# Performance work log

Hardware: AMD Instinct MI355X
Metric: run time of the kernel (lower is better)

## Reference

```python
import jax, jax.numpy as jnp
import numpy as np
import math

B, T, TE, D, H = 1, 2048, 1024, 1024, 16
HD = D // H
INF = 1e9  # infinity_proxy from the original module
INIT_SCALE = 0.02


def sinusoid_pos_emb(timesteps, dim):
    # Transformer-XL sinusoids for relative positions [timesteps-1 .. 0].
    inv_freq = 1.0 / (10000.0 ** (np.arange(0, dim, 2) / dim))
    pos_seq = np.arange(timesteps - 1, -1, -1.0)
    inp = np.einsum('i,j->ij', pos_seq, inv_freq)
    return np.concatenate([np.sin(inp), np.cos(inp)], axis=-1).astype(np.float32)


def relative_shift(x):
    # x: [b, h, t, T] -> TXL left-pad / reshape / slice shift trick.
    b, h, t1, t2 = x.shape
    x = jnp.pad(x, ((0, 0), (0, 0), (0, 0), (1, 0)))
    x = x.reshape(b, h, t2 + 1, t1)[:, :, 1:, :]
    return x.reshape(b, h, t1, t2)


def setup_inputs() -> dict:
    key = jax.random.key(0)
    ks = jax.random.split(key, 12)
    s = INIT_SCALE
    x = jax.random.normal(ks[0], (B, T, D), jnp.float32)
    extra = jax.random.normal(ks[1], (B, TE, D), jnp.float32)
    # causal mask over the in-sequence keys; full visibility on the extra memory
    mask = jnp.broadcast_to(jnp.tril(jnp.ones((T, T), jnp.float32))[None, None], (B, 1, T, T))
    extra_mask = jnp.ones((B, 1, T, TE), jnp.float32)
    Wq = jax.random.normal(ks[2], (D, D), jnp.float32) * s
    Wk = jax.random.normal(ks[3], (D, D), jnp.float32) * s
    Wv = jax.random.normal(ks[4], (D, D), jnp.float32) * s
    Wek = jax.random.normal(ks[5], (D, D), jnp.float32) * s
    Wev = jax.random.normal(ks[6], (D, D), jnp.float32) * s
    Wr = jax.random.normal(ks[7], (D, D), jnp.float32) * s
    Wo = jax.random.normal(ks[8], (D, D), jnp.float32) * s
    r_w_bias = jax.random.normal(ks[9], (H, HD), jnp.float32) * s
    r_r_bias = jax.random.normal(ks[10], (H, HD), jnp.float32) * s
    return dict(x=x, extra=extra, mask=mask, extra_mask=extra_mask,
                Wq=Wq, Wk=Wk, Wv=Wv, Wek=Wek, Wev=Wev, Wr=Wr, Wo=Wo,
                r_w_bias=r_w_bias, r_r_bias=r_r_bias)


def reference(x, extra, mask, extra_mask, Wq, Wk, Wv, Wek, Wev, Wr, Wo, r_w_bias, r_r_bias):
    b, t, d = x.shape
    te = extra.shape[1]
    # conv1d(kernel=1, no bias) == matmul projections; cache_steps=0 so y == x
    q = (x @ Wq).reshape(b, t, H, HD)
    k = (x @ Wk).reshape(b, t, H, HD)
    v = (x @ Wv).reshape(b, t, H, HD)
    # Transformer-XL relative-position attend_fn
    pos = jnp.asarray(sinusoid_pos_emb(t, d))            # [t, D]
    r = (pos @ Wr).reshape(t, H, HD)                      # [t, H, HD]
    content = jnp.einsum('bthd,bThd->bhtT', q + r_w_bias, k)
    rel = relative_shift(jnp.einsum('bthd,Thd->bhtT', q + r_r_bias, r))
    attn = content + rel
    attn = attn * mask - INF * (1.0 - mask)
    # extra keys/values use plain dot-product attention (no rel-pos)
    ek = (extra @ Wek).reshape(b, te, H, HD)
    ev = (extra @ Wev).reshape(b, te, H, HD)
    eattn = jnp.einsum('bthd,bThd->bhtT', q, ek)
    eattn = eattn * extra_mask - INF * (1.0 - extra_mask)
    attn = jnp.concatenate([attn, eattn], axis=-1) * (1.0 / math.sqrt(HD))
    p = jax.nn.softmax(attn, axis=-1)
    vv = jnp.concatenate([v, ev], axis=1)                 # [b, t+te, H, HD]
    out = jnp.einsum('bhtT,bThd->bthd', p, vv).reshape(b, t, d)
    return out @ Wo  # final conv1d, with_final_bias=False
```

## Files before the change

### kernel.cpp

```cpp
#include <hip/hip_runtime.h>
#include <hip/hip_bf16.h>
#include <math.h>

#define T_LEN 2048
#define TE_LEN 1024
#define D_DIM 1024
#define H_NUM 16
#define HD_DIM 64
#define R_PAD 64

typedef unsigned short ushort;
typedef __attribute__((ext_vector_type(8))) short short8;
typedef __attribute__((ext_vector_type(4))) float f32x4;
typedef __attribute__((ext_vector_type(4))) ushort ushort4v;

__device__ __forceinline__ ushort f2b(float f) {
    unsigned u = __builtin_bit_cast(unsigned, f);
    u += 0x7fffu + ((u >> 16) & 1u);
    return (ushort)(u >> 16);
}
__device__ __forceinline__ float b2f(ushort s) {
    unsigned u = ((unsigned)s) << 16;
    return __builtin_bit_cast(float, u);
}

__device__ __forceinline__ void gld16(const ushort* g, ushort* l) {
    __builtin_amdgcn_global_load_lds(
        (const __attribute__((address_space(1))) unsigned int*)g,
        (__attribute__((address_space(3))) unsigned int*)l, 16, 0, 0);
}

union U8 { short8 v; ushort u[8]; };

__global__ void prep_kernel(const float* __restrict__ x, const float* __restrict__ extra,
                            ushort* __restrict__ pos, ushort* __restrict__ xb,
                            ushort* __restrict__ eb) {
    const int q = blockIdx.x * 256 + threadIdx.x;
    const int PQ = 524288;
    const int XQ = 1048576;
    if (q < PQ) {
        int idx = q * 4;
        int i = idx >> 10, j = idx & 1023;
        bool sinreg = (j < 512);
        int jj = sinreg ? j : j - 512;
        float p = (float)(2047 - i);
        ushort4v o;
#pragma unroll
        for (int u = 0; u < 4; u++) {
            float inv = exp2f((float)(jj + u) * -0.025952563241f);
            float fa = p * inv;
            ((ushort*)&o)[u] = f2b(sinreg ? sinf(fa) : cosf(fa));
        }
        *(ushort4v*)&pos[idx] = o;
    } else if (q < XQ) {
        int idx = (q - PQ) * 4;
        float4 v = *(const float4*)&x[idx];
        ushort4v o = {f2b(v.x), f2b(v.y), f2b(v.z), f2b(v.w)};
        *(ushort4v*)&xb[idx] = o;
    } else {
        int idx = (q - XQ) * 4;
        float4 v = *(const float4*)&extra[idx];
        ushort4v o = {f2b(v.x), f2b(v.y), f2b(v.z), f2b(v.w)};
        *(ushort4v*)&eb[idx] = o;
    }
}

__global__ __launch_bounds__(256) void transpose7_kernel(
    const float* __restrict__ W0, const float* __restrict__ W1,
    const float* __restrict__ W2, const float* __restrict__ W3,
    const float* __restrict__ W4, const float* __restrict__ W5,
    const float* __restrict__ W6, ushort* __restrict__ out,
    ushort* __restrict__ Rpad) {
    if (blockIdx.z == 7) {
        int gid = (blockIdx.y * 32 + blockIdx.x) * 256 + threadIdx.x;
        if (gid < (R_PAD * 1024) / 8) {
            short8 z = {0, 0, 0, 0, 0, 0, 0, 0};
            *(short8*)&Rpad[gid * 8] = z;
        }
        return;
    }
    const float* Ws[7] = {W0, W1, W2, W3, W4, W5, W6};
    const float* W = Ws[blockIdx.z];
    ushort* WT = out + (size_t)blockIdx.z * (1024 * 1024);
    __shared__ float tile[32][33];
    int c0 = blockIdx.x * 32, r0 = blockIdx.y * 32;
    int tid = threadIdx.x;
#pragma unroll
    for (int p = 0; p < 4; p++) {
        int idx = tid + p * 256;
        int r = idx >> 5, c = idx & 31;
        tile[r][c] = W[(size_t)(r0 + r) * D_DIM + c0 + c];
    }
    __syncthreads();
#pragma unroll
    for (int p = 0; p < 4; p++) {
        int idx = tid + p * 256;
        int r = idx >> 5, c = idx & 31;
        WT[(size_t)(c0 + r) * D_DIM + r0 + c] = f2b(tile[c][r]);
    }
}

__global__ __launch_bounds__(256) void gemm_mega(
    const ushort* __restrict__ xb, const ushort* __restrict__ posb,
    const ushort* __restrict__ eb, const ushort* __restrict__ WT,
    ushort* __restrict__ Qb, ushort* __restrict__ Kb, ushort* __restrict__ VTb,
    ushort* __restrict__ Rb, ushort* __restrict__ EKb, ushort* __restrict__ EVTb) {
    __shared__ ushort As[128 * 64];
    __shared__ ushort Bs[128 * 64];
    const int tid = threadIdx.x;
    const int lane = tid & 63, w = tid >> 6;
    const int l15 = lane & 15, quad = lane >> 4;
    const int wm = w & 1, wn = w >> 1;
    const size_t M1 = 1024 * 1024;

    int idx = blockIdx.x;
    const ushort *A, *BT;
    ushort* dst;
    int m0, nb0, nc0, ldt = 1024;
    bool transp = false;
    if (idx < 384) {
        m0 = (idx & 15) * 128; nb0 = (idx >> 4) * 128;
        A = xb; BT = WT;
        nc0 = nb0 & 1023;
        int seg = nb0 >> 10;
        if (seg == 0) dst = Qb;
        else if (seg == 1) dst = Kb;
        else { dst = VTb; transp = true; ldt = T_LEN; }
    } else if (idx < 512) {
        int i = idx - 384;
        m0 = (i & 15) * 128; nb0 = (i >> 4) * 128; nc0 = nb0;
        A = posb; BT = WT + 5 * M1; dst = Rb;
    } else {
        int i = idx - 512;
        m0 = (i & 7) * 128; nb0 = (i >> 3) * 128; nc0 = nb0 & 1023;
        A = eb; BT = WT + 3 * M1;
        if (nb0 < 1024) dst = EKb;
        else { dst = EVTb; transp = true; ldt = TE_LEN; }
    }

    f32x4 acc[16];
#pragma unroll
    for (int i = 0; i < 16; i++) acc[i] = (f32x4){0.f, 0.f, 0.f, 0.f};

    for (int k0 = 0; k0 < 1024; k0 += 64) {
        __syncthreads();
#pragma unroll
        for (int i = 0; i < 4; i++) {
            int ci = i * 256 + tid;
            int row = ci >> 3, cs = (ci & 7) ^ (row & 7);
            gld16(A + (size_t)(m0 + row) * 1024 + k0 + cs * 8, &As[(i * 32 + w * 8) * 64]);
            gld16(BT + (size_t)(nb0 + row) * 1024 + k0 + cs * 8, &Bs[(i * 32 + w * 8) * 64]);
        }
        __syncthreads();
#pragma unroll
        for (int kc = 0; kc < 2; kc++) {
            short8 bfr[4];
#pragma unroll
            for (int nf = 0; nf < 4; nf++) {
                const int row = wn * 64 + nf * 16 + l15;
                bfr[nf] = *(const short8*)&Bs[(row * 8 + ((kc * 4 + quad) ^ (row & 7))) * 8];
            }
#pragma unroll
            for (int mf = 0; mf < 4; mf++) {
                const int row = wm * 64 + mf * 16 + l15;
                short8 afr = *(const short8*)&As[(row * 8 + ((kc * 4 + quad) ^ (row & 7))) * 8];
#pragma unroll
                for (int nf = 0; nf < 4; nf++)
                    acc[mf * 4 + nf] = __builtin_amdgcn_mfma_f32_16x16x32_bf16(afr, bfr[nf], acc[mf * 4 + nf], 0, 0, 0);
            }
        }
    }

#pragma unroll
    for (int mf = 0; mf < 4; mf++) {
#pragma unroll
        for (int nf = 0; nf < 4; nf++) {
            f32x4 a = acc[mf * 4 + nf];
            const int mrow = m0 + wm * 64 + mf * 16 + quad * 4;
            const int nc = nc0 + wn * 64 + nf * 16 + l15;
            if (transp) {
                ushort4v v = {f2b(a[0]), f2b(a[1]), f2b(a[2]), f2b(a[3])};
                *(ushort4v*)&dst[(size_t)nc * ldt + mrow] = v;
            } else {
#pragma unroll
                for (int r = 0; r < 4; r++) dst[(size_t)(mrow + r) * 1024 + nc] = f2b(a[r]);
            }
        }
    }
}

__global__ __launch_bounds__(256) void gemm_wo(const ushort* __restrict__ A,
                                               const ushort* __restrict__ BT,
                                               float* __restrict__ out) {
    __shared__ ushort As[128 * 64];
    __shared__ ushort Bs[64 * 64];
    const int tid = threadIdx.x;
    const int lane = tid & 63, w = tid >> 6;
    const int l15 = lane & 15, quad = lane >> 4;
    const int wm = w & 1, wn = w >> 1;
    const int m0 = blockIdx.y * 128, n0 = blockIdx.x * 64;

    f32x4 acc[8];
#pragma unroll
    for (int i = 0; i < 8; i++) acc[i] = (f32x4){0.f, 0.f, 0.f, 0.f};

    for (int k0 = 0; k0 < 1024; k0 += 64) {
        __syncthreads();
#pragma unroll
        for (int i = 0; i < 4; i++) {
            int ci = i * 256 + tid;
            int row = ci >> 3, cs = (ci & 7) ^ (row & 7);
            gld16(A + (size_t)(m0 + row) * 1024 + k0 + cs * 8, &As[(i * 32 + w * 8) * 64]);
        }
#pragma unroll
        for (int i = 0; i < 2; i++) {
            int ci = i * 256 + tid;
            int row = ci >> 3, cs = (ci & 7) ^ (row & 7);
            gld16(BT + (size_t)(n0 + row) * 1024 + k0 + cs * 8, &Bs[(i * 32 + w * 8) * 64]);
        }
        __syncthreads();
#pragma unroll
        for (int kc = 0; kc < 2; kc++) {
            short8 bfr[2];
#pragma unroll
            for (int nf = 0; nf < 2; nf++) {
                const int row = wn * 32 + nf * 16 + l15;
                bfr[nf] = *(const short8*)&Bs[(row * 8 + ((kc * 4 + quad) ^ (row & 7))) * 8];
            }
#pragma unroll
            for (int mf = 0; mf < 4; mf++) {
                const int row = wm * 64 + mf * 16 + l15;
                short8 afr = *(const short8*)&As[(row * 8 + ((kc * 4 + quad) ^ (row & 7))) * 8];
#pragma unroll
                for (int nf = 0; nf < 2; nf++)
                    acc[mf * 2 + nf] = __builtin_amdgcn_mfma_f32_16x16x32_bf16(afr, bfr[nf], acc[mf * 2 + nf], 0, 0, 0);
            }
        }
    }

#pragma unroll
    for (int mf = 0; mf < 4; mf++) {
#pragma unroll
        for (int nf = 0; nf < 2; nf++) {
            f32x4 a = acc[mf * 2 + nf];
            const int mrow = m0 + wm * 64 + mf * 16 + quad * 4;
            const int nc = n0 + wn * 32 + nf * 16 + l15;
#pragma unroll
            for (int r = 0; r < 4; r++) out[(size_t)(mrow + r) * 1024 + nc] = a[r];
        }
    }
}

__global__ __launch_bounds__(512) void attn_kernel(
    const ushort* __restrict__ Qb, const ushort* __restrict__ Kb,
    const ushort* __restrict__ VT, const ushort* __restrict__ Rb,
    const ushort* __restrict__ EKb, const ushort* __restrict__ EVT,
    const float* __restrict__ rwb, const float* __restrict__ rrb,
    ushort* __restrict__ AOb) {
    __shared__ __align__(16) ushort lds[37888];

    const int tid = threadIdx.x;
    const int lane = tid & 63, w = tid >> 6;
    const int g = w >> 2, wl = w & 3;
    const int gtid = tid & 255;
    const int l15 = lane & 15, quad = lane >> 4;
    const int blk = blockIdx.x;
    const int xcd = blk & 7, rnd = blk >> 8, slot = (blk >> 3) & 31;
    const int h = xcd * 2 + rnd;
    const int qt = rnd ? slot : 31 - slot;
    const int t0 = qt * 64, tf = t0 + wl * 16;
    const int hbase = h * HD_DIM;
    const int base0 = 1984 - t0;
    const int ninl = qt + 1;
    const int ntotl = ninl + 16;
    const int tt_s = g * ninl;
    const int baseg = base0 + 32 * tt_s;

    ushort* Kst = lds + g * 4096;
    ushort* Vst = lds + 8192 + g * 4096;
    ushort* Rst = lds + 16384 + g * 8192;
    ushort* Pw  = lds + 32768 + w * 640;

    short8 qw[2], qr[2], qp[2];
#pragma unroll
    for (int kh = 0; kh < 2; kh++) {
        int dof = hbase + kh * 32 + quad * 8;
        U8 raw; raw.v = *(const short8*)&Qb[(size_t)(tf + l15) * D_DIM + dof];
        U8 a, b, c;
#pragma unroll
        for (int j = 0; j < 8; j++) {
            float f = b2f(raw.u[j]);
            a.u[j] = f2b((f + rwb[dof + j]) * 0.125f);
            b.u[j] = f2b((f + rrb[dof + j]) * 0.125f);
            c.u[j] = f2b(f * 0.125f);
        }
        qw[kh] = a.v; qr[kh] = b.v; qp[kh] = c.v;
    }

    float lr[4] = {0.f, 0.f, 0.f, 0.f};
    f32x4 O[4];
#pragma unroll
    for (int i = 0; i < 4; i++) O[i] = (f32x4){0.f, 0.f, 0.f, 0.f};

    auto stageKV = [&](int i2, int buf) {
        const bool ins = i2 < ninl;
        const int j0 = ins ? (tt_s + i2) * 32 : (g * 16 + (i2 - ninl)) * 32;
        const ushort* ksrc = ins ? Kb : EKb;
        const ushort* vsrc = ins ? VT : EVT;
        const int ldv = ins ? T_LEN : TE_LEN;
        {
            int row = gtid >> 3, cs = (gtid & 7) ^ (row & 7);
            gld16(ksrc + (size_t)(j0 + row) * 1024 + hbase + cs * 8,
                  &Kst[buf * 2048 + wl * 512]);
        }
        {
            int row = gtid >> 2, cs = (gtid & 3) ^ (row & 3);
            gld16(vsrc + (size_t)(hbase + row) * ldv + j0 + cs * 8,
                  &Vst[buf * 2048 + wl * 512]);
        }
    };
    auto stageR = [&](int slotbase, int rowbase) {
        int k = gtid >> 3;
        int s = slotbase + k;
        int cs = (gtid & 7) ^ (s & 7);
        gld16(Rb + (size_t)(rowbase + k) * 1024 + hbase + cs * 8,
              &Rst[(slotbase + wl * 8) * 64]);
    };

#pragma unroll
    for (int i = 0; i < 3; i++) {
        int ci = i * 256 + gtid;
        int k = ci >> 3, cs = (ci & 7) ^ (k & 7);
        gld16(Rb + (size_t)(baseg + k) * 1024 + hbase + cs * 8,
              &Rst[(i * 32 + wl * 8) * 64]);
    }
    stageKV(0, 0);

    int srcA[4]; bool lowcA[4];
#pragma unroll
    for (int r = 0; r < 4; r++) {
        const int m = quad * 4 + r;
        const int cb = 15 - m + l15;
        srcA[r] = (lane & 48) | (cb & 15);
        lowcA[r] = (cb < 16);
    }

#pragma unroll 1
    for (int i = 0; i < ntotl; i++) {
        const int b = i & 1;
        __syncthreads();
        if (i + 1 < ntotl) {
            stageKV(i + 1, 1 - b);
            if (i + 1 < ninl) stageR((96 + 32 * i) & 127, baseg + 96 + 32 * i);
        }

        const bool ins = i < ninl;
        const int j0 = (tt_s + i) * 32;

        f32x4 con[2];
#pragma unroll
        for (int c = 0; c < 2; c++) con[c] = (f32x4){0.f, 0.f, 0.f, 0.f};
#pragma unroll
        for (int kh = 0; kh < 2; kh++) {
            const short8* qa = ins ? &qw[kh] : &qp[kh];
#pragma unroll
            for (int nh = 0; nh < 2; nh++) {
                const int row = nh * 16 + l15;
                short8 kf = *(const short8*)&Kst[b * 2048 + (row * 8 + ((kh * 4 + quad) ^ (row & 7))) * 8];
                con[nh] = __builtin_amdgcn_mfma_f32_16x16x32_bf16(*qa, kf, con[nh], 0, 0, 0);
            }
        }

        if (ins) {
            f32x4 rel[3];
#pragma unroll
            for (int c = 0; c < 3; c++) rel[c] = (f32x4){0.f, 0.f, 0.f, 0.f};
#pragma unroll
            for (int kh = 0; kh < 2; kh++)
#pragma unroll
                for (int cf = 0; cf < 3; cf++) {
                    const int s = (48 - 16 * wl + 32 * i + 16 * cf + l15) & 127;
                    short8 rf = *(const short8*)&Rst[(s * 8 + ((kh * 4 + quad) ^ (s & 7))) * 8];
                    rel[cf] = __builtin_amdgcn_mfma_f32_16x16x32_bf16(qr[kh], rf, rel[cf], 0, 0, 0);
                }
            const bool needmask = (j0 + 31 > tf);
#pragma unroll
            for (int r = 0; r < 4; r++) {
                const int m = quad * 4 + r;
                float b0 = __shfl(rel[0][r], srcA[r]);
                float b1 = __shfl(rel[1][r], srcA[r]);
                float b2 = __shfl(rel[2][r], srcA[r]);
                float rv0 = lowcA[r] ? b0 : b1, rv1 = lowcA[r] ? b1 : b2;
                float p0 = __expf(con[0][r] + rv0);
                float p1 = __expf(con[1][r] + rv1);
                if (needmask) {
                    const int t = tf + m;
                    if (j0 + l15 > t)      p0 = 0.f;
                    if (j0 + 16 + l15 > t) p1 = 0.f;
                }
                lr[r] += p0 + p1;
                Pw[m * 40 + l15]      = f2b(p0);
                Pw[m * 40 + 16 + l15] = f2b(p1);
            }
        } else {
#pragma unroll
            for (int r = 0; r < 4; r++) {
                const int m = quad * 4 + r;
                float p0 = __expf(con[0][r]);
                float p1 = __expf(con[1][r]);
                lr[r] += p0 + p1;
                Pw[m * 40 + l15]      = f2b(p0);
                Pw[m * 40 + 16 + l15] = f2b(p1);
            }
        }

        short8 pa = *(const short8*)&Pw[l15 * 40 + quad * 8];
#pragma unroll
        for (int df = 0; df < 4; df++) {
            const int row = df * 16 + l15;
            short8 vb = *(const short8*)&Vst[b * 2048 + (row * 4 + (quad ^ (row & 3))) * 8];
            O[df] = __builtin_amdgcn_mfma_f32_16x16x32_bf16(pa, vb, O[df], 0, 0, 0);
        }
    }

#pragma unroll
    for (int r = 0; r < 4; r++)
#pragma unroll
        for (int dd = 1; dd < 16; dd <<= 1) lr[r] += __shfl_xor(lr[r], dd);

    float* exch = (float*)(lds + 24576);
    float* exl  = (float*)(lds + 4096);
    __syncthreads();
    if (g == 1) {
#pragma unroll
        for (int r = 0; r < 4; r++) {
            const int row = wl * 16 + quad * 4 + r;
            if (l15 == 0) exl[row] = lr[r];
#pragma unroll
            for (int df = 0; df < 4; df++)
                exch[row * 65 + df * 16 + l15] = O[df][r];
        }
    }
    __syncthreads();
    if (g == 0) {
#pragma unroll
        for (int r = 0; r < 4; r++) {
            const int row = wl * 16 + quad * 4 + r;
            const float inv = 1.0f / (lr[r] + exl[row]);
#pragma unroll
            for (int df = 0; df < 4; df++)
                AOb[(size_t)(t0 + row) * D_DIM + hbase + df * 16 + l15] =
                    f2b((O[df][r] + exch[row * 65 + df * 16 + l15]) * inv);
        }
    }
}

extern "C" void kernel_launch(void* const* d_in, const int* in_sizes, int n_in,
                              void* d_out, int out_size, void* d_ws, size_t ws_size,
                              hipStream_t stream) {
    const float* x     = (const float*)d_in[0];
    const float* extra = (const float*)d_in[1];
    const float* Wq  = (const float*)d_in[4];
    const float* Wk  = (const float*)d_in[5];
    const float* Wv  = (const float*)d_in[6];
    const float* Wek = (const float*)d_in[7];
    const float* Wev = (const float*)d_in[8];
    const float* Wr  = (const float*)d_in[9];
    const float* Wo  = (const float*)d_in[10];
    const float* rwb = (const float*)d_in[11];
    const float* rrb = (const float*)d_in[12];
    float* out = (float*)d_out;

    ushort* ws = (ushort*)d_ws;
    const size_t M1 = 1024 * 1024;
    size_t o = 0;
    ushort* posb = ws + o; o += 2 * M1;
    ushort* xb   = ws + o; o += 2 * M1;
    ushort* eb   = ws + o; o += M1;
    ushort* WT   = ws + o; o += 7 * M1;
    ushort* Qb   = ws + o; o += 2 * M1;
    ushort* Kb   = ws + o; o += 2 * M1;
    ushort* VTb  = ws + o; o += 2 * M1;
    ushort* Rb   = ws + o; o += (size_t)(T_LEN + R_PAD) * 1024;
    ushort* EKb  = ws + o; o += M1;
    ushort* EVTb = ws + o; o += M1;
    ushort* AOb  = posb;

    prep_kernel<<<5120, 256, 0, stream>>>(x, extra, posb, xb, eb);
    transpose7_kernel<<<dim3(32, 32, 8), 256, 0, stream>>>(
        Wq, Wk, Wv, Wek, Wev, Wr, Wo, WT, Rb + (size_t)T_LEN * 1024);

    gemm_mega<<<640, 256, 0, stream>>>(xb, posb, eb, WT, Qb, Kb, VTb, Rb, EKb, EVTb);

    attn_kernel<<<512, 512, 0, stream>>>(Qb, Kb, VTb, Rb, EKb, EVTb, rwb, rrb, AOb);

    gemm_wo<<<dim3(16, 16), 256, 0, stream>>>(AOb, WT + 6 * M1, out);
}
```

Measured before the change: 272.1 us.

## Drop LDS staging of R, load R fragments from global and reuse overlapping tile

Removes the shared-memory ring buffer for the relative-position projection R, cutting LDS from about 74KB to about 42KB and adding a launch bound hint that targets higher occupancy. Each wave now loads its R fragments straight from global memory into registers. It also carries the third rel-score tile into the next iteration, since that tile overlaps the first tile of the next step, which cuts rel MFMAs from six to four per step. The cost is uncoalesced, unstaged global loads on the critical path and possible register pressure under the tighter launch bound.

Result: slower. 297.7 us (+9.4%).

```diff
diff --git a/kernel.cpp b/kernel.cpp
--- a/kernel.cpp
+++ b/kernel.cpp
@@ -251,13 +251,13 @@
     }
 }
 
-__global__ __launch_bounds__(512) void attn_kernel(
+__global__ __launch_bounds__(512, 4) void attn_kernel(
     const ushort* __restrict__ Qb, const ushort* __restrict__ Kb,
     const ushort* __restrict__ VT, const ushort* __restrict__ Rb,
     const ushort* __restrict__ EKb, const ushort* __restrict__ EVT,
     const float* __restrict__ rwb, const float* __restrict__ rrb,
     ushort* __restrict__ AOb) {
-    __shared__ __align__(16) ushort lds[37888];
+    __shared__ __align__(16) ushort lds[21504];
 
     const int tid = threadIdx.x;
     const int lane = tid & 63, w = tid >> 6;
@@ -278,8 +278,7 @@
 
     ushort* Kst = lds + g * 4096;
     ushort* Vst = lds + 8192 + g * 4096;
-    ushort* Rst = lds + 16384 + g * 8192;
-    ushort* Pw  = lds + 32768 + w * 640;
+    ushort* Pw  = lds + 16384 + w * 640;
 
     short8 qw[2], qr[2], qp[2];
 #pragma unroll
@@ -301,6 +300,7 @@
     f32x4 O[4];
 #pragma unroll
     for (int i = 0; i < 4; i++) O[i] = (f32x4){0.f, 0.f, 0.f, 0.f};
+    f32x4 rel_carry = (f32x4){0.f, 0.f, 0.f, 0.f};
 
     auto stageKV = [&](int i2, int buf) {
         const bool ins = i2 < ninl;
@@ -319,21 +319,7 @@
                   &Vst[buf * 2048 + wl * 512]);
         }
     };
-    auto stageR = [&](int slotbase, int rowbase) {
-        int k = gtid >> 3;
-        int s = slotbase + k;
-        int cs = (gtid & 7) ^ (s & 7);
-        gld16(Rb + (size_t)(rowbase + k) * 1024 + hbase + cs * 8,
-              &Rst[(slotbase + wl * 8) * 64]);
-    };
-
-#pragma unroll
-    for (int i = 0; i < 3; i++) {
-        int ci = i * 256 + gtid;
-        int k = ci >> 3, cs = (ci & 7) ^ (k & 7);
-        gld16(Rb + (size_t)(baseg + k) * 1024 + hbase + cs * 8,
-              &Rst[(i * 32 + wl * 8) * 64]);
-    }
+
     stageKV(0, 0);
 
     int srcA[4]; bool lowcA[4];
@@ -349,13 +335,26 @@
     for (int i = 0; i < ntotl; i++) {
         const int b = i & 1;
         __syncthreads();
-        if (i + 1 < ntotl) {
-            stageKV(i + 1, 1 - b);
-            if (i + 1 < ninl) stageR((96 + 32 * i) & 127, baseg + 96 + 32 * i);
-        }
+        if (i + 1 < ntotl) stageKV(i + 1, 1 - b);
 
         const bool ins = i < ninl;
         const int j0 = (tt_s + i) * 32;
+
+        short8 rf1[2], rf2[2], rf0[2];
+        if (ins) {
+            const size_t rbase =
+                (size_t)(baseg + 48 - 16 * wl + 32 * i + l15) * 1024 + hbase + quad * 8;
+#pragma unroll
+            for (int kh = 0; kh < 2; kh++) {
+                rf1[kh] = *(const short8*)&Rb[rbase + 16 * 1024 + kh * 32];
+                rf2[kh] = *(const short8*)&Rb[rbase + 32 * 1024 + kh * 32];
+            }
+            if (i == 0) {
+#pragma unroll
+                for (int kh = 0; kh < 2; kh++)
+                    rf0[kh] = *(const short8*)&Rb[rbase + kh * 32];
+            }
+        }
 
         f32x4 con[2];
 #pragma unroll
@@ -372,24 +371,31 @@
         }
 
         if (ins) {
-            f32x4 rel[3];
-#pragma unroll
-            for (int c = 0; c < 3; c++) rel[c] = (f32x4){0.f, 0.f, 0.f, 0.f};
-#pragma unroll
-            for (int kh = 0; kh < 2; kh++)
-#pragma unroll
-                for (int cf = 0; cf < 3; cf++) {
-                    const int s = (48 - 16 * wl + 32 * i + 16 * cf + l15) & 127;
-                    short8 rf = *(const short8*)&Rst[(s * 8 + ((kh * 4 + quad) ^ (s & 7))) * 8];
-                    rel[cf] = __builtin_amdgcn_mfma_f32_16x16x32_bf16(qr[kh], rf, rel[cf], 0, 0, 0);
-                }
+            f32x4 relA, rel1, rel2;
+            rel1 = (f32x4){0.f, 0.f, 0.f, 0.f};
+            rel2 = (f32x4){0.f, 0.f, 0.f, 0.f};
+            if (i == 0) {
+                relA = (f32x4){0.f, 0.f, 0.f, 0.f};
+#pragma unroll
+                for (int kh = 0; kh < 2; kh++)
+                    relA = __builtin_amdgcn_mfma_f32_16x16x32_bf16(qr[kh], rf0[kh], relA, 0, 0, 0);
+            } else {
+                relA = rel_carry;
+            }
+#pragma unroll
+            for (int kh = 0; kh < 2; kh++) {
+                rel1 = __builtin_amdgcn_mfma_f32_16x16x32_bf16(qr[kh], rf1[kh], rel1, 0, 0, 0);
+                rel2 = __builtin_amdgcn_mfma_f32_16x16x32_bf16(qr[kh], rf2[kh], rel2, 0, 0, 0);
+            }
+            rel_carry = rel2;
+
             const bool needmask = (j0 + 31 > tf);
 #pragma unroll
             for (int r = 0; r < 4; r++) {
                 const int m = quad * 4 + r;
-                float b0 = __shfl(rel[0][r], srcA[r]);
-                float b1 = __shfl(rel[1][r], srcA[r]);
-                float b2 = __shfl(rel[2][r], srcA[r]);
+                float b0 = __shfl(relA[r], srcA[r]);
+                float b1 = __shfl(rel1[r], srcA[r]);
+                float b2 = __shfl(rel2[r], srcA[r]);
                 float rv0 = lowcA[r] ? b0 : b1, rv1 = lowcA[r] ? b1 : b2;
                 float p0 = __expf(con[0][r] + rv0);
                 float p1 = __expf(con[1][r] + rv1);
@@ -428,8 +434,8 @@
 #pragma unroll
         for (int dd = 1; dd < 16; dd <<= 1) lr[r] += __shfl_xor(lr[r], dd);
 
-    float* exch = (float*)(lds + 24576);
-    float* exl  = (float*)(lds + 4096);
+    float* exch = (float*)(lds);
+    float* exl  = (float*)(lds + 12288);
     __syncthreads();
     if (g == 1) {
 #pragma unroll
```
